# Kernel optimization log

Hardware: AMD Instinct MI355X
Metric: run time of the kernel (lower is better)

Reference implementation:

```python
import jax, jax.numpy as jnp
import numpy as np

B, T, C = 4, 2048, 1024
NUM_HEADS, HEAD_DIM = 16, 64
INNER = NUM_HEADS * HEAD_DIM
OUT_DIM = 1024


def setup_inputs() -> dict:
    key = jax.random.key(0)
    kx, kk, kq, kv, kp = jax.random.split(key, 5)
    return {
        "x": jax.random.normal(kx, (B, T, C), dtype=jnp.float32),
        "W_k": jax.random.normal(kk, (INNER, C), dtype=jnp.float32),
        "W_q": jax.random.normal(kq, (INNER, C), dtype=jnp.float32),
        "W_v": jax.random.normal(kv, (INNER, C), dtype=jnp.float32),
        "W_p": jax.random.normal(kp, (OUT_DIM, INNER), dtype=jnp.float32),
    }


def reference(x, W_k, W_q, W_v, W_p):
    b, t, c = x.shape
    h, d = NUM_HEADS, HEAD_DIM
    scale_in = c ** (-0.5)
    # project and split heads: [B, H, T, D]
    def proj(W):
        y = jnp.einsum('btc,ic->bti', x, W) * scale_in
        return y.reshape(b, t, h, d).transpose(0, 2, 1, 3)
    k = proj(W_k)
    q = proj(W_q)
    v = proj(W_v)
    scores = jnp.einsum('bhqd,bhkd->bhqk', q, k) * (d ** (-0.5))
    weight = jax.nn.softmax(scores, axis=-1)
    out = jnp.einsum('bhqk,bhkd->bhqd', weight, v)  # [B,H,T,D]
    out = out.transpose(0, 2, 1, 3).reshape(b, t, h * d)
    out = jnp.einsum('bti,oi->bto', out, W_p) * (W_p.shape[-1] ** (-0.5))
    return out
```

## Files before the change

kernel.cpp:

```cpp
#include <hip/hip_runtime.h>
#include <math.h>

typedef __attribute__((ext_vector_type(8))) short bh8;
typedef __attribute__((ext_vector_type(4))) float f32x4;
typedef __attribute__((ext_vector_type(2))) unsigned u32x2;

namespace {
constexpr int Bn = 4, Tn = 2048, Cn = 1024, Hn = 16, Dn = 64, INNERn = 1024, OUTn = 1024;
constexpr int Mn = Bn * Tn;
}

__device__ __forceinline__ void glds16(const void* g, void* l) {
    __builtin_amdgcn_global_load_lds(
        (const __attribute__((address_space(1))) void*)g,
        (__attribute__((address_space(3))) void*)l, 16, 0, 0);
}

__device__ __forceinline__ void barrier_vm0() {
    __builtin_amdgcn_s_waitcnt(0x0070);
    __builtin_amdgcn_s_barrier();
}

__device__ __forceinline__ ushort f2bf(float f) {
    union { float f; unsigned u; } v; v.f = f;
    unsigned r = v.u + 0x7fffu + ((v.u >> 16) & 1u);
    return (ushort)(r >> 16);
}
__device__ __forceinline__ unsigned pack_rne(float a, float b) {
    return (unsigned)f2bf(a) | ((unsigned)f2bf(b) << 16);
}
__device__ __forceinline__ unsigned pack_trunc(float a, float b) {
    return __builtin_amdgcn_perm(__float_as_uint(a), __float_as_uint(b), 0x03020706u);
}

__global__ __launch_bounds__(256)
void cvt_all(const float* __restrict__ x,  const float* __restrict__ Wk,
             const float* __restrict__ Wq, const float* __restrict__ Wv,
             const float* __restrict__ Wp,
             ushort* __restrict__ xb,  ushort* __restrict__ wkb,
             ushort* __restrict__ wqb, ushort* __restrict__ wvb,
             ushort* __restrict__ wpb)
{
    const int bid = blockIdx.x;
    const float* s; ushort* d; float sc; int i;
    if (bid < 8192) {
        s = x; d = xb; sc = 0.03125f;
        i = bid * 256 + threadIdx.x;
    } else {
        const int seg = (bid - 8192) >> 10;
        i = ((bid - 8192) & 1023) * 256 + threadIdx.x;
        s  = (seg == 0) ? Wk : (seg == 1) ? Wq : (seg == 2) ? Wv : Wp;
        d  = (seg == 0) ? wkb : (seg == 1) ? wqb : (seg == 2) ? wvb : wpb;
        sc = (seg == 3) ? 0.03125f : 1.0f;
    }
    float4 f = ((const float4*)s)[i];
    ushort4 o;
    o.x = f2bf(f.x * sc); o.y = f2bf(f.y * sc);
    o.z = f2bf(f.z * sc); o.w = f2bf(f.w * sc);
    ((ushort4*)d)[i] = o;
}

__global__ __launch_bounds__(256)
void gemm_qkv(const ushort* __restrict__ A, const ushort* __restrict__ Wq,
              const ushort* __restrict__ Wk, const ushort* __restrict__ Wv,
              ushort* __restrict__ Oq, ushort* __restrict__ Ok,
              ushort* __restrict__ Ovt, float qscale)
{
    __shared__ char SM[32768];
    char* As0 = SM;          char* As1 = SM + 8192;
    char* Bs0 = SM + 16384;  char* Bs1 = SM + 24576;
    const int tid = threadIdx.x;
    const int w = tid >> 6, lane = tid & 63, quad = lane >> 4, l = lane & 15;
    const int lid = blockIdx.x;
    const int xcd = lid & 7, j = lid >> 3;
    const int ytile = xcd * 8 + j / 24;
    const int xx = j % 24;
    const int sel = xx >> 3;
    const ushort* Bw = (sel == 0) ? Wq : (sel == 1) ? Wk : Wv;
    const int n0 = (xx & 7) * 128, m0 = ytile * 128;
    const int wm = w >> 1, wn = w & 1;

    auto stage = [&](char* Ad, char* Bd, int k0) {
#pragma unroll
        for (int rr = 0; rr < 2; ++rr) {
            const int rho = w * 2 + rr;
            const int row = rho * 16 + (lane >> 2);
            const int kq  = (lane & 3) * 8;
            glds16(A  + (size_t)(m0 + row) * Cn + k0 + kq, Ad + rho * 1024 + lane * 16);
            glds16(Bw + (size_t)(n0 + row) * Cn + k0 + kq, Bd + rho * 1024 + lane * 16);
        }
    };

    f32x4 acc[4][4];
#pragma unroll
    for (int i = 0; i < 4; ++i)
#pragma unroll
        for (int j2 = 0; j2 < 4; ++j2) acc[i][j2] = (f32x4){0.f, 0.f, 0.f, 0.f};

    stage(As0, Bs0, 0);
    barrier_vm0();
#pragma unroll 2
    for (int it = 0; it < 32; ++it) {
        const int cur = it & 1;
        if (it < 31) stage(cur ? As0 : As1, cur ? Bs0 : Bs1, (it + 1) * 32);
        const char* Ac = cur ? As1 : As0; const char* Bc = cur ? Bs1 : Bs0;
        bh8 af[4], bf[4];
#pragma unroll
        for (int mf = 0; mf < 4; ++mf)
            af[mf] = *(const bh8*)(Ac + (wm * 64 + mf * 16 + l) * 64 + quad * 16);
#pragma unroll
        for (int nf = 0; nf < 4; ++nf)
            bf[nf] = *(const bh8*)(Bc + (wn * 64 + nf * 16 + l) * 64 + quad * 16);
#pragma unroll
        for (int mf = 0; mf < 4; ++mf)
#pragma unroll
            for (int nf = 0; nf < 4; ++nf)
                acc[mf][nf] = __builtin_amdgcn_mfma_f32_16x16x32_bf16(af[mf], bf[nf], acc[mf][nf], 0, 0, 0);
        barrier_vm0();
    }

    if (sel < 2) {
        ushort* dU = (sel == 0) ? Oq : Ok;
        const float scale = (sel == 0) ? qscale : 1.0f;
#pragma unroll
        for (int mf = 0; mf < 4; ++mf)
#pragma unroll
            for (int nf = 0; nf < 4; ++nf) {
                const int mb = m0 + wm * 64 + mf * 16 + quad * 4;
                const int n  = n0 + wn * 64 + nf * 16 + l;
                const int h = n >> 6, dd = n & 63;
#pragma unroll
                for (int reg = 0; reg < 4; ++reg) {
                    const int m = mb + reg;
                    const int b = m >> 11, t = m & (Tn - 1);
                    dU[((size_t)(b * Hn + h) * Tn + t) * Dn + dd] = f2bf(acc[mf][nf][reg] * scale);
                }
            }
    } else {
#pragma unroll
        for (int mf = 0; mf < 4; ++mf)
#pragma unroll
            for (int nf = 0; nf < 4; ++nf) {
                const int mb = wm * 64 + mf * 16 + quad * 4;
                const int n  = wn * 64 + nf * 16 + l;
                uint2 p;
                p.x = pack_rne(acc[mf][nf][0], acc[mf][nf][1]);
                p.y = pack_rne(acc[mf][nf][2], acc[mf][nf][3]);
                const int c = mb >> 3;
                *(uint2*)(SM + n * 256 + ((c ^ (n & 15)) & 15) * 16 + (mb & 7) * 2) = p;
            }
        __syncthreads();
        const int bb = m0 >> 11, t0 = m0 & (Tn - 1);
#pragma unroll
        for (int it2 = 0; it2 < 8; ++it2) {
            const int n = it2 * 16 + w * 4 + quad;
            const int ng = n0 + n;
            const int h = ng >> 6, dd = ng & 63;
            int4 vsm = *(const int4*)(SM + n * 256 + ((l ^ (n & 15)) & 15) * 16);
            *(int4*)(Ovt + ((size_t)(bb * Hn + h) * Dn + dd) * Tn + t0 + l * 8) = vsm;
        }
    }
}

__global__ __launch_bounds__(256)
void gemm_po(const ushort* __restrict__ A, const ushort* __restrict__ Bw,
             float* __restrict__ Cout)
{
    __shared__ char As[2][16384];
    __shared__ char Bs[2][16384];
    const int tid = threadIdx.x;
    const int w = tid >> 6, lane = tid & 63, quad = lane >> 4, l = lane & 15;
    const int lid = blockIdx.x;
    const int xcd = lid & 7, j = lid >> 3;
    const int n0 = (j & 7) * 128, m0 = (xcd * 8 + (j >> 3)) * 128;
    const int wm = w >> 1, wn = w & 1;

    auto stage = [&](int bsel, int k0) {
#pragma unroll
        for (int i = 0; i < 4; ++i) {
            const int c = tid + 256 * i;
            const int row = c >> 3, slot = c & 7;
            const int kc = slot ^ (row & 7);
            glds16(A  + (size_t)(m0 + row) * Cn + k0 + kc * 8, As[bsel] + c * 16);
            glds16(Bw + (size_t)(n0 + row) * Cn + k0 + kc * 8, Bs[bsel] + c * 16);
        }
    };

    f32x4 acc[4][4];
#pragma unroll
    for (int i = 0; i < 4; ++i)
#pragma unroll
        for (int j2 = 0; j2 < 4; ++j2) acc[i][j2] = (f32x4){0.f, 0.f, 0.f, 0.f};

    stage(0, 0);
    barrier_vm0();
#pragma unroll 2
    for (int it = 0; it < 16; ++it) {
        const int cur = it & 1;
        if (it < 15) stage(cur ^ 1, (it + 1) * 64);
        const char* Ac = As[cur]; const char* Bc = Bs[cur];
        bh8 af[4][2], bf[4][2];
#pragma unroll
        for (int mf = 0; mf < 4; ++mf) {
            const int row = wm * 64 + mf * 16 + l;
#pragma unroll
            for (int ks = 0; ks < 2; ++ks)
                af[mf][ks] = *(const bh8*)(Ac + row * 128 + (((ks * 4 + quad) ^ (l & 7)) * 16));
        }
#pragma unroll
        for (int nf = 0; nf < 4; ++nf) {
            const int row = wn * 64 + nf * 16 + l;
#pragma unroll
            for (int ks = 0; ks < 2; ++ks)
                bf[nf][ks] = *(const bh8*)(Bc + row * 128 + (((ks * 4 + quad) ^ (l & 7)) * 16));
        }
#pragma unroll
        for (int ks = 0; ks < 2; ++ks)
#pragma unroll
            for (int mf = 0; mf < 4; ++mf)
#pragma unroll
                for (int nf = 0; nf < 4; ++nf)
                    acc[mf][nf] = __builtin_amdgcn_mfma_f32_16x16x32_bf16(af[mf][ks], bf[nf][ks], acc[mf][nf], 0, 0, 0);
        barrier_vm0();
    }

#pragma unroll
    for (int mf = 0; mf < 4; ++mf)
#pragma unroll
        for (int nf = 0; nf < 4; ++nf) {
            const int mb = m0 + wm * 64 + mf * 16 + quad * 4;
            const int n  = n0 + wn * 64 + nf * 16 + l;
#pragma unroll
            for (int reg = 0; reg < 4; ++reg)
                Cout[(size_t)(mb + reg) * OUTn + n] = acc[mf][nf][reg];
        }
}

__global__ __launch_bounds__(256, 4)
void attn_mfma(const ushort* __restrict__ Qg, const ushort* __restrict__ Kg,
               const ushort* __restrict__ Vtg, ushort* __restrict__ Og)
{
    __shared__ char KT[2][8192];
    __shared__ char VT[2][8192];

    const int tid = threadIdx.x;
    const int w = tid >> 6, lane = tid & 63, quad = lane >> 4, l = lane & 15;
    const int lid = blockIdx.x;
    const int xcd = lid & 7, j = lid >> 3;
    const int bh = (xcd << 3) | (j >> 4);
    const int q0 = (j & 15) * 128;
    const int b = bh >> 4, h = bh & 15;
    const ushort* Qp = Qg  + (size_t)bh * Tn * Dn;
    const ushort* Kp = Kg  + (size_t)bh * Tn * Dn;
    const ushort* Vp = Vtg + (size_t)bh * Dn * Tn;

    auto stageK = [&](char* buf, int kt) {
#pragma unroll
        for (int rr = 0; rr < 2; ++rr) {
            const int rho = w * 2 + rr;
            const int r8  = lane >> 3;
            const int r   = rho * 8 + r8;
            const int dc  = (lane & 7) ^ r8;
            glds16(Kp + (size_t)(kt * 64 + r) * Dn + dc * 8, buf + rho * 1024 + lane * 16);
        }
    };
    auto stageV = [&](char* buf, int kt) {
#pragma unroll
        for (int rr = 0; rr < 2; ++rr) {
            const int rho = w * 2 + rr;
            const int d = rho * 8 + (lane >> 3);
            const int csrc = (lane & 7) ^ ((lane >> 3) & 7);
            glds16(Vp + (size_t)d * Tn + kt * 64 + csrc * 8, buf + rho * 1024 + lane * 16);
        }
    };

    bh8 qf[2][2];
#pragma unroll
    for (int nt = 0; nt < 2; ++nt)
#pragma unroll
        for (int ks = 0; ks < 2; ++ks)
            qf[nt][ks] = *(const bh8*)(Qp + (size_t)(q0 + w * 32 + nt * 16 + l) * Dn + ks * 32 + quad * 8);

    bh8 ones;
#pragma unroll
    for (int i = 0; i < 8; ++i) ones[i] = (short)0x3F80;

    f32x4 oacc[2][4], lacc[2];
#pragma unroll
    for (int nt = 0; nt < 2; ++nt) {
        lacc[nt] = (f32x4){0.f, 0.f, 0.f, 0.f};
#pragma unroll
        for (int dt = 0; dt < 4; ++dt) oacc[nt][dt] = (f32x4){0.f, 0.f, 0.f, 0.f};
    }

    const f32x4 zero = (f32x4){0.f, 0.f, 0.f, 0.f};

    stageK(KT[0], 0);
    stageV(VT[0], 0);
    barrier_vm0();

#pragma unroll 2
    for (int kt = 0; kt < Tn / 64; ++kt) {
        const int cur = kt & 1;
        if (kt < Tn / 64 - 1) {
            stageK(KT[cur ^ 1], kt + 1);
            stageV(VT[cur ^ 1], kt + 1);
        }
        const char* Kc = KT[cur];
        const char* Vc = VT[cur];

#pragma unroll
        for (int hh = 0; hh < 2; ++hh) {
            bh8 kf[2][2];
#pragma unroll
            for (int k8l = 0; k8l < 2; ++k8l) {
                const int row = (hh * 2 + k8l) * 16 + l;
#pragma unroll
                for (int ks = 0; ks < 2; ++ks)
                    kf[k8l][ks] = *(const bh8*)(Kc + row * 128 + (((ks * 4 + quad) ^ (l & 7)) * 16));
            }

            f32x4 st[2][2];
            __builtin_amdgcn_s_setprio(1);
#pragma unroll
            for (int nt = 0; nt < 2; ++nt)
#pragma unroll
                for (int k8l = 0; k8l < 2; ++k8l) {
                    st[nt][k8l] = __builtin_amdgcn_mfma_f32_16x16x32_bf16(kf[k8l][0], qf[nt][0], zero, 0, 0, 0);
                    st[nt][k8l] = __builtin_amdgcn_mfma_f32_16x16x32_bf16(kf[k8l][1], qf[nt][1], st[nt][k8l], 0, 0, 0);
                }
            __builtin_amdgcn_s_setprio(0);

            bh8 pf[2];
#pragma unroll
            for (int nt = 0; nt < 2; ++nt) {
                const unsigned a0 = pack_trunc(__builtin_amdgcn_exp2f(st[nt][0][0]),
                                               __builtin_amdgcn_exp2f(st[nt][0][1]));
                const unsigned a1 = pack_trunc(__builtin_amdgcn_exp2f(st[nt][0][2]),
                                               __builtin_amdgcn_exp2f(st[nt][0][3]));
                const unsigned b0 = pack_trunc(__builtin_amdgcn_exp2f(st[nt][1][0]),
                                               __builtin_amdgcn_exp2f(st[nt][1][1]));
                const unsigned b1 = pack_trunc(__builtin_amdgcn_exp2f(st[nt][1][2]),
                                               __builtin_amdgcn_exp2f(st[nt][1][3]));
                const u32x2 p = __builtin_amdgcn_permlane32_swap(a0, b0, false, false);
                const u32x2 q = __builtin_amdgcn_permlane16_swap(p.x, p.y, false, false);
                const u32x2 r = __builtin_amdgcn_permlane32_swap(a1, b1, false, false);
                const u32x2 s = __builtin_amdgcn_permlane16_swap(r.x, r.y, false, false);
                union { unsigned u[4]; bh8 v; } pu;
                pu.u[0] = q.x; pu.u[1] = s.x; pu.u[2] = q.y; pu.u[3] = s.y;
                pf[nt] = pu.v;
            }

            bh8 vf[4];
#pragma unroll
            for (int dt = 0; dt < 4; ++dt)
                vf[dt] = *(const bh8*)(Vc + (dt * 16 + l) * 128 + (((hh * 4 + quad) ^ (l & 7)) * 16));
            __builtin_amdgcn_s_setprio(1);
#pragma unroll
            for (int nt = 0; nt < 2; ++nt)
                lacc[nt] = __builtin_amdgcn_mfma_f32_16x16x32_bf16(ones, pf[nt], lacc[nt], 0, 0, 0);
#pragma unroll
            for (int dt = 0; dt < 4; ++dt)
#pragma unroll
                for (int nt = 0; nt < 2; ++nt)
                    oacc[nt][dt] = __builtin_amdgcn_mfma_f32_16x16x32_bf16(vf[dt], pf[nt], oacc[nt][dt], 0, 0, 0);
            __builtin_amdgcn_s_setprio(0);
        }
        barrier_vm0();
    }

#pragma unroll
    for (int nt = 0; nt < 2; ++nt) {
        const float inv = 1.0f / lacc[nt][0];
        const int t = q0 + w * 32 + nt * 16 + l;
#pragma unroll
        for (int dt = 0; dt < 4; ++dt) {
            uint2 p;
            p.x = pack_rne(oacc[nt][dt][0] * inv, oacc[nt][dt][1] * inv);
            p.y = pack_rne(oacc[nt][dt][2] * inv, oacc[nt][dt][3] * inv);
            *(uint2*)(Og + ((size_t)(b * Tn + t)) * INNERn + h * 64 + dt * 16 + quad * 4) = p;
        }
    }
}

extern "C" void kernel_launch(void* const* d_in, const int* in_sizes, int n_in,
                              void* d_out, int out_size, void* d_ws, size_t ws_size,
                              hipStream_t stream)
{
    const float* x  = (const float*)d_in[0];
    const float* Wk = (const float*)d_in[1];
    const float* Wq = (const float*)d_in[2];
    const float* Wv = (const float*)d_in[3];
    const float* Wp = (const float*)d_in[4];
    float* out = (float*)d_out;

    ushort* xb  = (ushort*)d_ws;
    ushort* wkb = xb  + (size_t)Mn * Cn;
    ushort* wqb = wkb + (size_t)INNERn * Cn;
    ushort* wvb = wqb + (size_t)INNERn * Cn;
    ushort* wpb = wvb + (size_t)INNERn * Cn;
    ushort* qw  = wpb + (size_t)OUTn * INNERn;
    ushort* kw  = qw  + (size_t)Mn * INNERn;
    ushort* vtw = kw  + (size_t)Mn * INNERn;
    ushort* aow = vtw + (size_t)Mn * INNERn;

    const dim3 blk(256);
    cvt_all<<<dim3(8192 + 4096), blk, 0, stream>>>(x, Wk, Wq, Wv, Wp,
                                                   xb, wkb, wqb, wvb, wpb);

    gemm_qkv<<<dim3(1536), blk, 0, stream>>>(xb, wqb, wkb, wvb,
                                             qw, kw, vtw, 0.125f * 1.44269504f);

    attn_mfma<<<dim3(1024), blk, 0, stream>>>(qw, kw, vtw, aow);

    gemm_po<<<dim3(512), blk, 0, stream>>>(aow, wpb, out);
}
```

Before: 255.4 us.

## Fuse fp32-to-bf16 conversion of x into QKV GEMM A-tile staging

Drops the separate conversion pass over x. The QKV GEMM now loads fp32 x directly into registers, scales and rounds it to bf16, and writes it into the shared-memory A tile after the MFMA step, prefetching one stage ahead. This removes a full write and read of the bf16 copy of x plus one kernel's worth of work. In exchange, every column tile re-reads fp32 x (twice the bytes of bf16), and per-iteration conversion ALU work and register pressure are added.

```diff
diff --git a/kernel.cpp b/kernel.cpp
--- a/kernel.cpp
+++ b/kernel.cpp
@@ -34,25 +34,17 @@
 }
 
 __global__ __launch_bounds__(256)
-void cvt_all(const float* __restrict__ x,  const float* __restrict__ Wk,
-             const float* __restrict__ Wq, const float* __restrict__ Wv,
-             const float* __restrict__ Wp,
-             ushort* __restrict__ xb,  ushort* __restrict__ wkb,
-             ushort* __restrict__ wqb, ushort* __restrict__ wvb,
-             ushort* __restrict__ wpb)
+void cvt_w(const float* __restrict__ Wk, const float* __restrict__ Wq,
+           const float* __restrict__ Wv, const float* __restrict__ Wp,
+           ushort* __restrict__ wkb, ushort* __restrict__ wqb,
+           ushort* __restrict__ wvb, ushort* __restrict__ wpb)
 {
     const int bid = blockIdx.x;
-    const float* s; ushort* d; float sc; int i;
-    if (bid < 8192) {
-        s = x; d = xb; sc = 0.03125f;
-        i = bid * 256 + threadIdx.x;
-    } else {
-        const int seg = (bid - 8192) >> 10;
-        i = ((bid - 8192) & 1023) * 256 + threadIdx.x;
-        s  = (seg == 0) ? Wk : (seg == 1) ? Wq : (seg == 2) ? Wv : Wp;
-        d  = (seg == 0) ? wkb : (seg == 1) ? wqb : (seg == 2) ? wvb : wpb;
-        sc = (seg == 3) ? 0.03125f : 1.0f;
-    }
+    const int seg = bid >> 10;
+    const int i = (bid & 1023) * 256 + threadIdx.x;
+    const float* s = (seg == 0) ? Wk : (seg == 1) ? Wq : (seg == 2) ? Wv : Wp;
+    ushort* d = (seg == 0) ? wkb : (seg == 1) ? wqb : (seg == 2) ? wvb : wpb;
+    const float sc = (seg == 3) ? 0.03125f : 1.0f;
     float4 f = ((const float4*)s)[i];
     ushort4 o;
     o.x = f2bf(f.x * sc); o.y = f2bf(f.y * sc);
@@ -61,7 +53,7 @@
 }
 
 __global__ __launch_bounds__(256)
-void gemm_qkv(const ushort* __restrict__ A, const ushort* __restrict__ Wq,
+void gemm_qkv(const float* __restrict__ X, const ushort* __restrict__ Wq,
               const ushort* __restrict__ Wk, const ushort* __restrict__ Wv,
               ushort* __restrict__ Oq, ushort* __restrict__ Ok,
               ushort* __restrict__ Ovt, float qscale)
@@ -80,16 +72,34 @@
     const int n0 = (xx & 7) * 128, m0 = ytile * 128;
     const int wm = w >> 1, wn = w & 1;
 
-    auto stage = [&](char* Ad, char* Bd, int k0) {
+    auto stage_load = [&](int t, float4 (&av)[2][2]) {
+        char* Bd = (t & 1) ? Bs1 : Bs0;
 #pragma unroll
         for (int rr = 0; rr < 2; ++rr) {
             const int rho = w * 2 + rr;
             const int row = rho * 16 + (lane >> 2);
             const int kq  = (lane & 3) * 8;
-            glds16(A  + (size_t)(m0 + row) * Cn + k0 + kq, Ad + rho * 1024 + lane * 16);
-            glds16(Bw + (size_t)(n0 + row) * Cn + k0 + kq, Bd + rho * 1024 + lane * 16);
+            const float* src = X + (size_t)(m0 + row) * Cn + t * 32 + kq;
+            av[rr][0] = *(const float4*)(src);
+            av[rr][1] = *(const float4*)(src + 4);
+            glds16(Bw + (size_t)(n0 + row) * Cn + t * 32 + kq, Bd + rho * 1024 + lane * 16);
         }
     };
+    auto stage_write = [&](int t, const float4 (&av)[2][2]) {
+        char* Ad = (t & 1) ? As1 : As0;
+#pragma unroll
+        for (int rr = 0; rr < 2; ++rr) {
+            const int rho = w * 2 + rr;
+            const float* p0 = (const float*)&av[rr][0];
+            const float* p1 = (const float*)&av[rr][1];
+            int4 v;
+            v.x = pack_rne(p0[0] * 0.03125f, p0[1] * 0.03125f);
+            v.y = pack_rne(p0[2] * 0.03125f, p0[3] * 0.03125f);
+            v.z = pack_rne(p1[0] * 0.03125f, p1[1] * 0.03125f);
+            v.w = pack_rne(p1[2] * 0.03125f, p1[3] * 0.03125f);
+            *(int4*)(Ad + rho * 1024 + lane * 16) = v;
+        }
+    };
 
     f32x4 acc[4][4];
 #pragma unroll
@@ -97,12 +107,17 @@
 #pragma unroll
         for (int j2 = 0; j2 < 4; ++j2) acc[i][j2] = (f32x4){0.f, 0.f, 0.f, 0.f};
 
-    stage(As0, Bs0, 0);
+    {
+        float4 av0[2][2];
+        stage_load(0, av0);
+        stage_write(0, av0);
+    }
     barrier_vm0();
+    float4 avn[2][2];
 #pragma unroll 2
     for (int it = 0; it < 32; ++it) {
         const int cur = it & 1;
-        if (it < 31) stage(cur ? As0 : As1, cur ? Bs0 : Bs1, (it + 1) * 32);
+        if (it < 31) stage_load(it + 1, avn);
         const char* Ac = cur ? As1 : As0; const char* Bc = cur ? Bs1 : Bs0;
         bh8 af[4], bf[4];
 #pragma unroll
@@ -116,6 +131,7 @@
 #pragma unroll
             for (int nf = 0; nf < 4; ++nf)
                 acc[mf][nf] = __builtin_amdgcn_mfma_f32_16x16x32_bf16(af[mf], bf[nf], acc[mf][nf], 0, 0, 0);
+        if (it < 31) stage_write(it + 1, avn);
         barrier_vm0();
     }
 
@@ -394,8 +410,7 @@
     const float* Wp = (const float*)d_in[4];
     float* out = (float*)d_out;
 
-    ushort* xb  = (ushort*)d_ws;
-    ushort* wkb = xb  + (size_t)Mn * Cn;
+    ushort* wkb = (ushort*)d_ws;
     ushort* wqb = wkb + (size_t)INNERn * Cn;
     ushort* wvb = wqb + (size_t)INNERn * Cn;
     ushort* wpb = wvb + (size_t)INNERn * Cn;
@@ -405,10 +420,9 @@
     ushort* aow = vtw + (size_t)Mn * INNERn;
 
     const dim3 blk(256);
-    cvt_all<<<dim3(8192 + 4096), blk, 0, stream>>>(x, Wk, Wq, Wv, Wp,
-                                                   xb, wkb, wqb, wvb, wpb);
-
-    gemm_qkv<<<dim3(1536), blk, 0, stream>>>(xb, wqb, wkb, wvb,
+    cvt_w<<<dim3(4096), blk, 0, stream>>>(Wk, Wq, Wv, Wp, wkb, wqb, wvb, wpb);
+
+    gemm_qkv<<<dim3(1536), blk, 0, stream>>>(x, wqb, wkb, wvb,
                                              qw, kw, vtw, 0.125f * 1.44269504f);
 
     attn_mfma<<<dim3(1024), blk, 0, stream>>>(qw, kw, vtw, aow);
```

New measurement: 297.2 us. +16.4%, slower.
